# Kernel tuning notes

Hardware: AMD Instinct MI355X
Metric: run time of the kernel (lower is better)

The kernel has to match this reference:

```python
import jax, jax.numpy as jnp
import numpy as np

SEQ, BATCH = 1024, 2
N_HEAD, D_MODEL = 16, 1024
Q_LORA, KV_LORA = 20, 20
ROPE = D_MODEL // N_HEAD // 2   # 32 qk_rope_head_dim
NOPE = D_MODEL // N_HEAD // 2   # 32 qk_nope_head_dim
V_DIM = D_MODEL // N_HEAD       # 64
N_EXP, HID = 4, 1024            # hidden_dim = d_inner//5 = 5120//5
N_GROUP, TOPK_GROUP, TOP_K = 2, 2, 1
ROUTED_SCALE = 1.0


def setup_inputs() -> dict:
    key = jax.random.key(0)
    ks = jax.random.split(key, 16)
    sc = 0.02
    return {
        'dec_inp': jax.random.normal(ks[0], (SEQ, BATCH, D_MODEL), jnp.float32),
        'wq_a': jax.random.normal(ks[1], (D_MODEL, Q_LORA), jnp.float32) * sc,
        'q_norm_w': jnp.ones((Q_LORA,), jnp.float32),
        'wq_b': jax.random.normal(ks[2], (Q_LORA, N_HEAD * (NOPE + ROPE)), jnp.float32) * sc,
        'wkv_a': jax.random.normal(ks[3], (D_MODEL, KV_LORA + ROPE), jnp.float32) * sc,
        'kv_norm_w': jnp.ones((KV_LORA,), jnp.float32),
        'wkv_b': jax.random.normal(ks[4], (KV_LORA, N_HEAD * (NOPE + V_DIM)), jnp.float32) * sc,
        'wo': jax.random.normal(ks[5], (N_HEAD * V_DIM, D_MODEL), jnp.float32) * sc,
        'gate_w': jax.random.normal(ks[6], (N_EXP, D_MODEL), jnp.float32) * sc,
        'exp_gate': jax.random.normal(ks[7], (N_EXP, D_MODEL, HID), jnp.float32) * sc,
        'exp_up': jax.random.normal(ks[8], (N_EXP, D_MODEL, HID), jnp.float32) * sc,
        'exp_down': jax.random.normal(ks[9], (N_EXP, HID, D_MODEL), jnp.float32) * sc,
        'sh_gate': jax.random.normal(ks[10], (D_MODEL, HID), jnp.float32) * sc,
        'sh_up': jax.random.normal(ks[11], (D_MODEL, HID), jnp.float32) * sc,
        'sh_down': jax.random.normal(ks[12], (HID, D_MODEL), jnp.float32) * sc,
    }


def _rms(x, w, eps=1e-6):
    return x * jax.lax.rsqrt(jnp.mean(x * x, axis=-1, keepdims=True) + eps) * w


def _freqs(seqlen):
    # precompute_freqs_cis(rope_dim * n_head, seqlen): dim = 512 here
    dim = ROPE * N_HEAD
    inv = 1.0 / (10000.0 ** (jnp.arange(0, dim, 2, dtype=jnp.float32) / dim))  # [dim//2]
    ang = jnp.arange(seqlen, dtype=jnp.float32)[:, None] * inv[None, :]       # [s, dim//2]
    ang = ang.reshape(seqlen, N_HEAD, ROPE // 2)
    return jnp.cos(ang), jnp.sin(ang)


def _rope(x, cos, sin):
    # x: [b, s, h, ROPE]; interleaved-pair complex rotation
    b, s, h, _ = x.shape
    xr = x.reshape(b, s, h, ROPE // 2, 2)
    x0, x1 = xr[..., 0], xr[..., 1]
    c = cos[None]  # [1, s, h, ROPE//2]
    sn = sin[None]
    o0 = x0 * c - x1 * sn
    o1 = x0 * sn + x1 * c
    return jnp.stack([o0, o1], axis=-1).reshape(b, s, h, ROPE)


def reference(dec_inp, wq_a, q_norm_w, wq_b, wkv_a, kv_norm_w, wkv_b, wo,
              gate_w, exp_gate, exp_up, exp_down, sh_gate, sh_up, sh_down):
    x = jnp.swapaxes(dec_inp, 0, 1)  # [b, s, d]
    b, s, d = x.shape
    # ---- MLA attention ----
    q = _rms(x @ wq_a, q_norm_w) @ wq_b                       # [b, s, h*(nope+rope)]
    q = q.reshape(b, s, N_HEAD, NOPE + ROPE)
    q_nope, q_pe = q[..., :NOPE], q[..., NOPE:]
    kv = x @ wkv_a                                            # [b, s, kv_lora+rope]
    ckv, k_pe = kv[..., :KV_LORA], kv[..., KV_LORA:]
    kvb = (_rms(ckv, kv_norm_w) @ wkv_b).reshape(b, s, N_HEAD, NOPE + V_DIM)
    k_nope, v = kvb[..., :NOPE], kvb[..., NOPE:]
    cos, sin = _freqs(s)
    q_pe = _rope(q_pe, cos, sin)
    k_pe_h = _rope(jnp.broadcast_to(k_pe[:, :, None, :], (b, s, N_HEAD, ROPE)), cos, sin)
    qf = jnp.concatenate([q_nope, q_pe], axis=-1)             # [b, s, h, 64]
    kf = jnp.concatenate([k_nope, k_pe_h], axis=-1)
    scale = 1.0 / np.sqrt(NOPE + ROPE)
    scores = jnp.einsum('bshd,bthd->bhst', qf, kf) * scale    # mask=None in the source forward
    probs = jax.nn.softmax(scores, axis=-1)
    attn = jnp.einsum('bhst,bthd->bshd', probs, v).reshape(b, s, N_HEAD * V_DIM)
    y = attn @ wo                                             # [b, s, d]
    y = jnp.swapaxes(y, 0, 1)                                 # [s, b, d]
    # ---- DeepSeekMoE (group_limited_greedy, top_k=1, 1 shared expert) ----
    xf = y.reshape(-1, d)                                     # [T, d]
    T = xf.shape[0]
    sc = jax.nn.softmax(xf @ gate_w.T, axis=-1)               # [T, E]
    gsc = sc.reshape(T, N_GROUP, N_EXP // N_GROUP).max(axis=-1)  # [T, n_group]
    _, gidx = jax.lax.top_k(gsc, TOPK_GROUP)
    gmask = jax.nn.one_hot(gidx, N_GROUP, dtype=sc.dtype).sum(axis=1)  # [T, n_group]
    smask = jnp.repeat(gmask, N_EXP // N_GROUP, axis=-1)      # [T, E]
    tw, ti = jax.lax.top_k(jnp.where(smask > 0, sc, 0.0), TOP_K)
    comb = (jax.nn.one_hot(ti, N_EXP, dtype=sc.dtype) * tw[..., None]).sum(axis=1) * ROUTED_SCALE  # [T, E]
    g = jnp.einsum('td,edh->teh', xf, exp_gate)
    u = jnp.einsum('td,edh->teh', xf, exp_up)
    dn = jnp.einsum('teh,ehd->ted', jax.nn.silu(g) * u, exp_down)
    routed = jnp.einsum('ted,te->td', dn, comb)
    shared = (jax.nn.silu(xf @ sh_gate) * (xf @ sh_up)) @ sh_down
    return (routed + shared).reshape(s, b, d)
```

## Files before the change

### kernel.cpp

```cpp
#include <hip/hip_runtime.h>
#include <hip/hip_bf16.h>
#include <math.h>

#define SEQ 1024
#define BATCH 2
#define T 2048
#define DM 1024
#define NH 16
#define NOPE 32
#define HD 64
#define QL 20
#define KVL 20
#define KVA 52
#define HID 1024
#define NEXP 4
#define LSTR 80

typedef short bf16x8 __attribute__((ext_vector_type(8)));
typedef float f32x4 __attribute__((ext_vector_type(4)));
typedef float f32x16 __attribute__((ext_vector_type(16)));
typedef __hip_bfloat16 bf16;

static __device__ __forceinline__ float sigmoidf_(float x) {
    return 1.0f / (1.0f + __expf(-x));
}
static __device__ __forceinline__ unsigned short bfbits(float x) {
    bf16 h = __float2bfloat16(x);
    return *reinterpret_cast<unsigned short*>(&h);
}
static __device__ __forceinline__ unsigned cvt_pk_bf16(float lo, float hi) {
    unsigned r;
    asm("v_cvt_pk_bf16_f32 %0, %1, %2" : "=v"(r) : "v"(lo), "v"(hi));
    return r;
}

__global__ __launch_bounds__(256) void k_setup(
    const float* __restrict__ wo, const float* __restrict__ sg,
    const float* __restrict__ su, const float* __restrict__ sd,
    const float* __restrict__ eg, const float* __restrict__ eu,
    const float* __restrict__ ed,
    bf16* __restrict__ woT, bf16* __restrict__ sgT, bf16* __restrict__ suT,
    bf16* __restrict__ sdT, bf16* __restrict__ egT, bf16* __restrict__ euT,
    bf16* __restrict__ edT,
    const float* __restrict__ wq_a, const float* __restrict__ wkv_a,
    const float* __restrict__ wq_b, const float* __restrict__ wkv_b,
    bf16* __restrict__ loraT, bf16* __restrict__ wqbT, bf16* __restrict__ wkvbT,
    float* __restrict__ ctab, float* __restrict__ stab)
{
    int z = blockIdx.z;
    int tid = threadIdx.x;
    if (z < 16) {
        __shared__ float tile[32][33];
        const float* in; bf16* out;
        if      (z == 0) { in = wo; out = woT; }
        else if (z == 1) { in = sg; out = sgT; }
        else if (z == 2) { in = su; out = suT; }
        else if (z == 3) { in = sd; out = sdT; }
        else if (z < 8)  { size_t o = (size_t)(z - 4)  * DM * HID; in = eg + o; out = egT + o; }
        else if (z < 12) { size_t o = (size_t)(z - 8)  * DM * HID; in = eu + o; out = euT + o; }
        else             { size_t o = (size_t)(z - 12) * HID * DM; in = ed + o; out = edT + o; }
        int c0 = blockIdx.x * 32, r0 = blockIdx.y * 32;
        int tx = tid & 31, ty = tid >> 5;
        #pragma unroll
        for (int ii = 0; ii < 4; ++ii)
            tile[ty + ii * 8][tx] = in[(size_t)(r0 + ty + ii * 8) * 1024 + c0 + tx];
        __syncthreads();
        int c = tid >> 3, rg = (tid & 7) * 4;
        ushort4 o4;
        o4.x = bfbits(tile[rg + 0][c]);
        o4.y = bfbits(tile[rg + 1][c]);
        o4.z = bfbits(tile[rg + 2][c]);
        o4.w = bfbits(tile[rg + 3][c]);
        *(ushort4*)&out[(size_t)(c0 + c) * 1024 + r0 + rg] = o4;
    } else if (z == 16) {
        int s = blockIdx.y * 32 + blockIdx.x;
        int p = tid;
        float freq = exp2f(-(float)p * (13.287712379549449f / 256.0f));
        float ang = (float)s * freq;
        float sn, cs;
        __sincosf(ang, &sn, &cs);
        ctab[s * 256 + p] = cs;
        stab[s * 256 + p] = sn;
    } else {
        int idx = (blockIdx.y * 32 + blockIdx.x) * 256 + tid;
        if (z == 17) {
            if (idx >= 80 * 1024) return;
            int n = idx >> 10, k = idx & 1023;
            float v = (n < 20) ? wq_a[k * QL + n] : (n < 72 ? wkv_a[k * KVA + (n - 20)] : 0.f);
            loraT[idx] = __float2bfloat16(v);
        } else if (z == 18) {
            if (idx >= 1024 * 32) return;
            int n = idx >> 5, k = idx & 31;
            wqbT[idx] = __float2bfloat16(k < 20 ? wq_b[k * DM + n] : 0.f);
        } else {
            if (idx >= 1536 * 32) return;
            int n = idx >> 5, k = idx & 31;
            wkvbT[idx] = __float2bfloat16(k < 20 ? wkv_b[k * (NH * 96) + n] : 0.f);
        }
    }
}

__global__ __launch_bounds__(256) void k_p1(
    const float* __restrict__ dec, const bf16* __restrict__ loraT,
    float* __restrict__ lora4)
{
    __shared__ __align__(16) char As[128 * LSTR];
    __shared__ __align__(16) char Bs[80 * LSTR];
    const int tid = threadIdx.x;
    const int kz = blockIdx.x;
    const int m0 = blockIdx.y * 128;
    const int lane = tid & 63, wave = tid >> 6;
    const int g = lane >> 4, c = lane & 15;
    f32x4 acc[2][5] = {};
    for (int ks = 0; ks < 16; ++ks) {
        int k0 = kz * 512 + ks * 32;
        __syncthreads();
        #pragma unroll
        for (int pass = 0; pass < 4; ++pass) {
            int row = (tid >> 3) + pass * 32;
            int t = m0 + row;
            int b = t >> 10, s = t & 1023;
            f32x4 v = *(const f32x4*)&dec[(size_t)(s * 2 + b) * DM + k0 + (tid & 7) * 4];
            ushort4 h4;
            h4.x = bfbits(v[0]); h4.y = bfbits(v[1]);
            h4.z = bfbits(v[2]); h4.w = bfbits(v[3]);
            *(ushort4*)&As[row * LSTR + (tid & 7) * 8] = h4;
        }
        if (tid < 160) {
            int row = tid >> 1, hf = tid & 1;
            const bf16* src = &loraT[row * 1024 + k0 + hf * 16];
            *(int4*)&Bs[row * LSTR + hf * 32]      = *(const int4*)&src[0];
            *(int4*)&Bs[row * LSTR + hf * 32 + 16] = *(const int4*)&src[8];
        }
        __syncthreads();
        bf16x8 af[2], bff[5];
        #pragma unroll
        for (int mi = 0; mi < 2; ++mi)
            af[mi] = *(const bf16x8*)&As[(wave * 32 + mi * 16 + c) * LSTR + 16 * g];
        #pragma unroll
        for (int nf = 0; nf < 5; ++nf)
            bff[nf] = *(const bf16x8*)&Bs[(nf * 16 + c) * LSTR + 16 * g];
        #pragma unroll
        for (int mi = 0; mi < 2; ++mi)
            #pragma unroll
            for (int nf = 0; nf < 5; ++nf)
                acc[mi][nf] = __builtin_amdgcn_mfma_f32_16x16x32_bf16(af[mi], bff[nf], acc[mi][nf], 0, 0, 0);
    }
    #pragma unroll
    for (int mi = 0; mi < 2; ++mi)
        #pragma unroll
        for (int nf = 0; nf < 5; ++nf)
            #pragma unroll
            for (int r = 0; r < 4; ++r) {
                int col = nf * 16 + c;
                if (col < 72) {
                    int row = m0 + wave * 32 + mi * 16 + 4 * g + r;
                    lora4[((size_t)kz * T + row) * 72 + col] = acc[mi][nf][r];
                }
            }
}

__global__ __launch_bounds__(256) void k_p2(
    const float* __restrict__ lora4, const float* __restrict__ qnw,
    const float* __restrict__ kvnw, bf16* __restrict__ nrmq, bf16* __restrict__ nrmkv,
    int* __restrict__ cnt)
{
    if (blockIdx.x == 0 && threadIdx.x < 16) cnt[threadIdx.x] = 0;
    int t = blockIdx.x * 256 + threadIdx.x;
    float lq[20], lk[20];
    float ssq = 0.f, ssk = 0.f;
    #pragma unroll
    for (int i = 0; i < 20; ++i) {
        lq[i] = lora4[t * 72 + i] + lora4[(size_t)(T + t) * 72 + i];
        ssq += lq[i] * lq[i];
    }
    #pragma unroll
    for (int i = 0; i < 20; ++i) {
        lk[i] = lora4[t * 72 + 20 + i] + lora4[(size_t)(T + t) * 72 + 20 + i];
        ssk += lk[i] * lk[i];
    }
    float fq = rsqrtf(ssq / 20.f + 1e-6f);
    float fk = rsqrtf(ssk / 20.f + 1e-6f);
    #pragma unroll
    for (int i = 0; i < 32; ++i) {
        nrmq[t * 32 + i]  = __float2bfloat16(i < 20 ? lq[i] * fq * qnw[i]  : 0.f);
        nrmkv[t * 32 + i] = __float2bfloat16(i < 20 ? lk[i] * fk * kvnw[i] : 0.f);
    }
}

__global__ __launch_bounds__(256) void k_p2b(
    const float* __restrict__ lora4, const float* __restrict__ ctab,
    const float* __restrict__ stab, bf16* __restrict__ kb)
{
    int t = blockIdx.x, p = threadIdx.x;
    int r = p & 15, h = p >> 4, s = t & (SEQ - 1);
    float y0 = lora4[t * 72 + 40 + 2 * r] + lora4[(size_t)(T + t) * 72 + 40 + 2 * r];
    float y1 = lora4[t * 72 + 41 + 2 * r] + lora4[(size_t)(T + t) * 72 + 41 + 2 * r];
    float cs = ctab[s * 256 + p], sn = stab[s * 256 + p];
    ushort2 pk;
    pk.x = bfbits(y0 * cs - y1 * sn);
    pk.y = bfbits(y0 * sn + y1 * cs);
    *(ushort2*)&kb[(size_t)t * DM + h * HD + NOPE + 2 * r] = pk;
}

__global__ __launch_bounds__(256) void k_p3q(
    const bf16* __restrict__ nrmq, const bf16* __restrict__ wqbT,
    const float* __restrict__ ctab, const float* __restrict__ stab,
    bf16* __restrict__ qb)
{
    __shared__ __align__(16) char As[128 * LSTR];
    __shared__ __align__(16) char Bs[64 * LSTR];
    const int tid = threadIdx.x;
    const int m0 = blockIdx.y * 128, n0 = blockIdx.x * 64;
    const int lane = tid & 63, wave = tid >> 6;
    const int g = lane >> 4, c = lane & 15;
    const int wm = wave >> 1, wn = wave & 1;
    {
        int row = tid >> 1, hf = tid & 1;
        const bf16* sa = &nrmq[(size_t)(m0 + row) * 32 + hf * 16];
        *(int4*)&As[row * LSTR + hf * 32]      = *(const int4*)&sa[0];
        *(int4*)&As[row * LSTR + hf * 32 + 16] = *(const int4*)&sa[8];
        int brow = tid >> 2;
        *(int4*)&Bs[brow * LSTR + (tid & 3) * 16] = *(const int4*)&wqbT[(size_t)(n0 + brow) * 32 + (tid & 3) * 8];
    }
    __syncthreads();
    f32x4 acc[4][2] = {};
    bf16x8 af[4], bfr[2];
    #pragma unroll
    for (int mi = 0; mi < 4; ++mi)
        af[mi] = *(const bf16x8*)&As[(wm * 64 + mi * 16 + c) * LSTR + 16 * g];
    #pragma unroll
    for (int ni = 0; ni < 2; ++ni)
        bfr[ni] = *(const bf16x8*)&Bs[(wn * 32 + ni * 16 + c) * LSTR + 16 * g];
    #pragma unroll
    for (int mi = 0; mi < 4; ++mi)
        #pragma unroll
        for (int ni = 0; ni < 2; ++ni) {
            acc[mi][ni] = __builtin_amdgcn_mfma_f32_16x16x32_bf16(af[mi], bfr[ni], acc[mi][ni], 0, 0, 0);
            #pragma unroll
            for (int r = 0; r < 4; ++r) acc[mi][ni][r] *= 0.18033688f;
        }

    #pragma unroll
    for (int mi = 0; mi < 4; ++mi)
        #pragma unroll
        for (int ni = 0; ni < 2; ++ni) {
            int n = n0 + wn * 32 + ni * 16 + c;
            int w = n & 63;
            if (w < 32) {
                #pragma unroll
                for (int r = 0; r < 4; ++r) {
                    int row = m0 + wm * 64 + mi * 16 + 4 * g + r;
                    qb[(size_t)row * DM + n] = __float2bfloat16(acc[mi][ni][r]);
                }
            } else {
                int h = n >> 6;
                int pidx = h * 16 + ((w - 32) >> 1);
                int odd = w & 1;
                #pragma unroll
                for (int r = 0; r < 4; ++r) {
                    int row = m0 + wm * 64 + mi * 16 + 4 * g + r;
                    int s = row & (SEQ - 1);
                    float own = acc[mi][ni][r];
                    float oth = __shfl_xor(own, 1);
                    float cs = ctab[s * 256 + pidx], sn = stab[s * 256 + pidx];
                    float o = odd ? (oth * sn + own * cs) : (own * cs - oth * sn);
                    qb[(size_t)row * DM + n] = __float2bfloat16(o);
                }
            }
        }
}

__global__ __launch_bounds__(256) void k_p3kv(
    const bf16* __restrict__ nrmkv, const bf16* __restrict__ wkvbT,
    bf16* __restrict__ kb, bf16* __restrict__ vt_g)
{
    __shared__ __align__(16) char As[128 * LSTR];
    __shared__ __align__(16) char Bs[64 * LSTR];
    const int tid = threadIdx.x;
    const int m0 = blockIdx.y * 128, n0 = blockIdx.x * 64;
    const int lane = tid & 63, wave = tid >> 6;
    const int g = lane >> 4, c = lane & 15;
    const int wm = wave >> 1, wn = wave & 1;
    {
        int row = tid >> 1, hf = tid & 1;
        const bf16* sa = &nrmkv[(size_t)(m0 + row) * 32 + hf * 16];
        *(int4*)&As[row * LSTR + hf * 32]      = *(const int4*)&sa[0];
        *(int4*)&As[row * LSTR + hf * 32 + 16] = *(const int4*)&sa[8];
        int brow = tid >> 2;
        *(int4*)&Bs[brow * LSTR + (tid & 3) * 16] = *(const int4*)&wkvbT[(size_t)(n0 + brow) * 32 + (tid & 3) * 8];
    }
    __syncthreads();
    f32x4 acc[4][2] = {};
    bf16x8 af[4], bfr[2];
    #pragma unroll
    for (int mi = 0; mi < 4; ++mi)
        af[mi] = *(const bf16x8*)&As[(wm * 64 + mi * 16 + c) * LSTR + 16 * g];
    #pragma unroll
    for (int ni = 0; ni < 2; ++ni)
        bfr[ni] = *(const bf16x8*)&Bs[(wn * 32 + ni * 16 + c) * LSTR + 16 * g];
    #pragma unroll
    for (int mi = 0; mi < 4; ++mi)
        #pragma unroll
        for (int ni = 0; ni < 2; ++ni)
            acc[mi][ni] = __builtin_amdgcn_mfma_f32_16x16x32_bf16(af[mi], bfr[ni], acc[mi][ni], 0, 0, 0);

    #pragma unroll
    for (int mi = 0; mi < 4; ++mi)
        #pragma unroll
        for (int ni = 0; ni < 2; ++ni) {
            int n = n0 + wn * 32 + ni * 16 + c;
            int h = n / 96, w = n - h * 96;
            int row0 = m0 + wm * 64 + mi * 16 + 4 * g;
            if (w < NOPE) {
                #pragma unroll
                for (int r = 0; r < 4; ++r)
                    kb[(size_t)(row0 + r) * DM + h * HD + w] = __float2bfloat16(acc[mi][ni][r]);
            } else {
                int d = w - NOPE;
                int b = row0 >> 10, s0 = row0 & (SEQ - 1);
                ushort4 v4;
                v4.x = bfbits(acc[mi][ni][0]);
                v4.y = bfbits(acc[mi][ni][1]);
                v4.z = bfbits(acc[mi][ni][2]);
                v4.w = bfbits(acc[mi][ni][3]);
                *(ushort4*)&vt_g[(((size_t)(b * NH + h) * HD + d) << 10) + s0] = v4;
            }
        }
}

__global__ __launch_bounds__(256) void k_attn(
    const bf16* __restrict__ qb, const bf16* __restrict__ kb,
    const bf16* __restrict__ vt_g, bf16* __restrict__ ab)
{
    __shared__ __align__(16) char stage[2][16384];
    __shared__ float pol[2][32][65];
    __shared__ float mll[2][32][2];

    const int qt = blockIdx.x, h = blockIdx.y, b = blockIdx.z;
    const int tid = threadIdx.x;
    const int lane = tid & 63, wave = tid >> 6;
    const int l31 = lane & 31, hi = lane >> 5;
    const int sp = wave >> 1, wq = wave & 1;
    const int q0 = qt * 64 + wq * 32;
    char* ks = stage[sp];
    char* vt = stage[sp] + 8192;
    const int ptid = tid & 127;

    bf16x8 qf[4];
    {
        const bf16* qrow = &qb[(size_t)(b * SEQ + q0 + l31) * DM + h * HD + 8 * hi];
        #pragma unroll
        for (int st = 0; st < 4; ++st)
            qf[st] = *(const bf16x8*)&qrow[16 * st];
    }

    f32x16 o0 = {}, o1 = {};
    float m_run = -3.0e38f, l_run = 0.f;
    const size_t vbase = ((size_t)(b * NH + h) * HD) << 10;

    for (int ktl = 0; ktl < 8; ++ktl) {
        const int kt = sp * 8 + ktl;
        __syncthreads();
        #pragma unroll
        for (int ps = 0; ps < 4; ++ps) {
            int row = (ptid >> 3) + ps * 16;
            int col8 = (ptid & 7) * 8;
            int sw = (col8 * 2) ^ ((row & 7) << 4);
            int4 kv4 = *(const int4*)&kb[(size_t)(b * SEQ + kt * 64 + row) * DM + h * HD + col8];
            *(int4*)&ks[row * 128 + sw] = kv4;
            int4 vv4 = *(const int4*)&vt_g[vbase + ((size_t)row << 10) + kt * 64 + col8];
            *(int4*)&vt[row * 128 + sw] = vv4;
        }
        __syncthreads();

        f32x16 sc0 = {}, sc1 = {};
        #pragma unroll
        for (int st = 0; st < 4; ++st) {
            int colb = 32 * st + 16 * hi;
            int r0 = l31;
            bf16x8 kf0 = *(const bf16x8*)&ks[r0 * 128 + (colb ^ ((r0 & 7) << 4))];
            sc0 = __builtin_amdgcn_mfma_f32_32x32x16_bf16(kf0, qf[st], sc0, 0, 0, 0);
            int r1 = 32 + l31;
            bf16x8 kf1 = *(const bf16x8*)&ks[r1 * 128 + (colb ^ ((r1 & 7) << 4))];
            sc1 = __builtin_amdgcn_mfma_f32_32x32x16_bf16(kf1, qf[st], sc1, 0, 0, 0);
        }

        float mt = fmaxf(sc0[0], sc1[0]);
        #pragma unroll
        for (int i = 1; i < 16; ++i) mt = fmaxf(mt, fmaxf(sc0[i], sc1[i]));
        mt = fmaxf(mt, __shfl_xor(mt, 32));

        if (!__all(mt <= m_run + 8.0f)) {
            float m_new = fmaxf(m_run, mt);
            float corr = exp2f(m_run - m_new);
            m_run = m_new;
            l_run *= corr;
            #pragma unroll
            for (int i = 0; i < 16; ++i) { o0[i] *= corr; o1[i] *= corr; }
        }
        float ls = 0.f;
        #pragma unroll
        for (int i = 0; i < 16; ++i) {
            sc0[i] = exp2f(sc0[i] - m_run);
            sc1[i] = exp2f(sc1[i] - m_run);
            ls += sc0[i] + sc1[i];
        }
        ls += __shfl_xor(ls, 32);
        l_run += ls;

        unsigned pk0[8], pk1[8];
        #pragma unroll
        for (int i = 0; i < 8; ++i) {
            pk0[i] = cvt_pk_bf16(sc0[2 * i], sc0[2 * i + 1]);
            pk1[i] = cvt_pk_bf16(sc1[2 * i], sc1[2 * i + 1]);
        }

#define PV_SUB(PK, KK)                                                          \
        {                                                                       \
            _Pragma("unroll")                                                   \
            for (int s = 0; s < 2; ++s) {                                       \
                unsigned sx = hi ? PK[4*s]   : PK[4*s+2];                       \
                unsigned rx = __shfl_xor(sx, 32);                               \
                unsigned sy = hi ? PK[4*s+1] : PK[4*s+3];                       \
                unsigned ry = __shfl_xor(sy, 32);                               \
                int4 bi;                                                        \
                bi.x = hi ? (int)rx : (int)PK[4*s];                             \
                bi.y = hi ? (int)ry : (int)PK[4*s+1];                           \
                bi.z = hi ? (int)PK[4*s+2] : (int)rx;                           \
                bi.w = hi ? (int)PK[4*s+3] : (int)ry;                           \
                bf16x8 bfr = *(bf16x8*)&bi;                                     \
                int cb = (KK) * 64 + 32 * s + 16 * hi;                          \
                {                                                               \
                    int vr = l31;                                               \
                    bf16x8 vf = *(const bf16x8*)&vt[vr * 128 + (cb ^ ((vr & 7) << 4))]; \
                    o0 = __builtin_amdgcn_mfma_f32_32x32x16_bf16(vf, bfr, o0, 0, 0, 0); \
                }                                                               \
                {                                                               \
                    int vr = 32 + l31;                                          \
                    bf16x8 vf = *(const bf16x8*)&vt[vr * 128 + (cb ^ ((vr & 7) << 4))]; \
                    o1 = __builtin_amdgcn_mfma_f32_32x32x16_bf16(vf, bfr, o1, 0, 0, 0); \
                }                                                               \
            }                                                                   \
        }
        PV_SUB(pk0, 0)
        PV_SUB(pk1, 1)
#undef PV_SUB
    }

    if (sp == 1) {
        #pragma unroll
        for (int i = 0; i < 16; ++i) {
            int d = (i & 3) + 8 * (i >> 2) + 4 * hi;
            pol[wq][l31][d]      = o0[i];
            pol[wq][l31][32 + d] = o1[i];
        }
        if (hi == 0) { mll[wq][l31][0] = m_run; mll[wq][l31][1] = l_run; }
    }
    __syncthreads();
    if (sp == 1) return;

    float m_b = mll[wq][l31][0], l_b = mll[wq][l31][1];
    float M = fmaxf(m_run, m_b);
    float wa = exp2f(m_run - M), wb = exp2f(m_b - M);
    float inv = 1.0f / (l_run * wa + l_b * wb);
    #pragma unroll
    for (int i = 0; i < 16; ++i) {
        int d = (i & 3) + 8 * (i >> 2) + 4 * hi;
        o0[i] = (o0[i] * wa + pol[wq][l31][d]      * wb) * inv;
        o1[i] = (o1[i] * wa + pol[wq][l31][32 + d] * wb) * inv;
    }

    char* tb = stage[wq];
    #pragma unroll
    for (int i = 0; i < 8; ++i) {
        int dbase = 2 * (i & 1) + 8 * (i >> 1) + 4 * hi;
        *(unsigned*)&tb[l31 * 140 + (dbase) * 2]      = cvt_pk_bf16(o0[2 * i], o0[2 * i + 1]);
        *(unsigned*)&tb[l31 * 140 + (32 + dbase) * 2] = cvt_pk_bf16(o1[2 * i], o1[2 * i + 1]);
    }
    __builtin_amdgcn_s_waitcnt(0);
    #pragma unroll
    for (int p = 0; p < 8; ++p) {
        int idx = p * 64 + lane;
        int q = idx >> 4, c8 = idx & 15;
        int2 rv;
        rv.x = *(const int*)&tb[q * 140 + c8 * 8];
        rv.y = *(const int*)&tb[q * 140 + c8 * 8 + 4];
        *(int2*)&ab[(size_t)(b * SEQ + q0 + q) * DM + h * HD + c8 * 4] = rv;
    }
}

__global__ __launch_bounds__(512) void k_mm_plain(
    const bf16* __restrict__ A, const bf16* __restrict__ Bt, bf16* __restrict__ C)
{
    __shared__ __align__(16) char As[128 * LSTR];
    __shared__ __align__(16) char Bs[64 * LSTR];
    const int tid = threadIdx.x;
    const int lane = tid & 63, wave = tid >> 6;
    const int g = lane >> 4, c = lane & 15;
    const int wm = wave >> 1, wn = wave & 1;
    const int m0 = blockIdx.y * 128, n0 = blockIdx.x * 64;
    const int sr = tid >> 2, sb = (tid & 3) * 16, scol = (tid & 3) * 8;
    const int srb = (tid & 255) >> 2;

    size_t aoff = (size_t)(m0 + sr) * DM + scol;
    size_t boff = (size_t)(n0 + srb) * DM + scol;
    int4 a0 = *(const int4*)&A[aoff];
    int4 b0;
    if (tid < 256) b0 = *(const int4*)&Bt[boff];

    f32x4 acc[2][2] = {};
    for (int k0 = 0; k0 < DM; k0 += 32) {
        __syncthreads();
        *(int4*)&As[sr * LSTR + sb] = a0;
        if (tid < 256) *(int4*)&Bs[srb * LSTR + sb] = b0;
        __syncthreads();
        if (k0 + 32 < DM) {
            a0 = *(const int4*)&A[aoff + k0 + 32];
            if (tid < 256) b0 = *(const int4*)&Bt[boff + k0 + 32];
        }
        bf16x8 af[2], bfx[2];
        #pragma unroll
        for (int mi = 0; mi < 2; ++mi)
            af[mi] = *(const bf16x8*)&As[(wm * 32 + mi * 16 + c) * LSTR + 16 * g];
        #pragma unroll
        for (int ni = 0; ni < 2; ++ni)
            bfx[ni] = *(const bf16x8*)&Bs[(wn * 32 + ni * 16 + c) * LSTR + 16 * g];
        #pragma unroll
        for (int mi = 0; mi < 2; ++mi)
            #pragma unroll
            for (int ni = 0; ni < 2; ++ni)
                acc[mi][ni] = __builtin_amdgcn_mfma_f32_16x16x32_bf16(af[mi], bfx[ni], acc[mi][ni], 0, 0, 0);
    }
    #pragma unroll
    for (int mi = 0; mi < 2; ++mi)
        #pragma unroll
        for (int ni = 0; ni < 2; ++ni)
            #pragma unroll
            for (int r = 0; r < 4; ++r)
                C[(size_t)(m0 + wm * 32 + mi * 16 + 4 * g + r) * DM + n0 + wn * 32 + ni * 16 + c]
                    = __float2bfloat16(acc[mi][ni][r]);
}

template<bool ROUTED>
__global__ __launch_bounds__(512) void k_mm_gu(
    const bf16* __restrict__ X, const bf16* __restrict__ BgT,
    const bf16* __restrict__ BuT, const int* __restrict__ cnt,
    const int* __restrict__ lists, bf16* __restrict__ act)
{
    const int e = blockIdx.z;
    const int ntok = ROUTED ? cnt[e] : T;
    const int m0 = blockIdx.y * 128;
    if (m0 >= ntok) return;
    const int n0 = blockIdx.x * 64;
    __shared__ __align__(16) char As[128 * LSTR];
    __shared__ __align__(16) char Bg[64 * LSTR];
    __shared__ __align__(16) char Bu[64 * LSTR];
    __shared__ int rowid[128];
    const int tid = threadIdx.x;
    if (tid < 128) {
        int idx = m0 + tid;
        rowid[tid] = ROUTED ? lists[e * T + (idx < ntok ? idx : ntok - 1)] : idx;
    }
    __syncthreads();
    const int lane = tid & 63, wave = tid >> 6;
    const int g = lane >> 4, c = lane & 15;
    const int wm = wave >> 1, wn = wave & 1;
    const int sr = tid >> 2, sb = (tid & 3) * 16, scol = (tid & 3) * 8;
    const int srb = (tid & 255) >> 2;
    const int ra = rowid[sr];
    const bf16* Bge = BgT + (ROUTED ? (size_t)e * HID * DM : 0);
    const bf16* Bue = BuT + (ROUTED ? (size_t)e * HID * DM : 0);
    const bf16* Bmine = (tid < 256) ? Bge : Bue;
    size_t aoff = (size_t)ra * DM + scol;
    size_t boff = (size_t)(n0 + srb) * DM + scol;
    int4 a0 = *(const int4*)&X[aoff];
    int4 b0 = *(const int4*)&Bmine[boff];
    char* Bdst = (tid < 256) ? Bg : Bu;

    f32x4 accg[2][2] = {}, accu[2][2] = {};
    for (int k0 = 0; k0 < DM; k0 += 32) {
        __syncthreads();
        *(int4*)&As[sr * LSTR + sb] = a0;
        *(int4*)&Bdst[srb * LSTR + sb] = b0;
        __syncthreads();
        if (k0 + 32 < DM) {
            a0 = *(const int4*)&X[aoff + k0 + 32];
            b0 = *(const int4*)&Bmine[boff + k0 + 32];
        }
        bf16x8 af[2], gf[2], uf[2];
        #pragma unroll
        for (int mi = 0; mi < 2; ++mi)
            af[mi] = *(const bf16x8*)&As[(wm * 32 + mi * 16 + c) * LSTR + 16 * g];
        #pragma unroll
        for (int ni = 0; ni < 2; ++ni) {
            gf[ni] = *(const bf16x8*)&Bg[(wn * 32 + ni * 16 + c) * LSTR + 16 * g];
            uf[ni] = *(const bf16x8*)&Bu[(wn * 32 + ni * 16 + c) * LSTR + 16 * g];
        }
        #pragma unroll
        for (int mi = 0; mi < 2; ++mi)
            #pragma unroll
            for (int ni = 0; ni < 2; ++ni) {
                accg[mi][ni] = __builtin_amdgcn_mfma_f32_16x16x32_bf16(af[mi], gf[ni], accg[mi][ni], 0, 0, 0);
                accu[mi][ni] = __builtin_amdgcn_mfma_f32_16x16x32_bf16(af[mi], uf[ni], accu[mi][ni], 0, 0, 0);
            }
    }
    #pragma unroll
    for (int mi = 0; mi < 2; ++mi)
        #pragma unroll
        for (int ni = 0; ni < 2; ++ni)
            #pragma unroll
            for (int r = 0; r < 4; ++r) {
                int lr = wm * 32 + mi * 16 + 4 * g + r;
                if (ROUTED && m0 + lr >= ntok) continue;
                int token = rowid[lr];
                float gv = accg[mi][ni][r], uv = accu[mi][ni][r];
                act[(size_t)token * HID + n0 + wn * 32 + ni * 16 + c] =
                    __float2bfloat16(gv * sigmoidf_(gv) * uv);
            }
}

template<bool ROUTED>
__global__ __launch_bounds__(512) void k_mm_down(
    const bf16* __restrict__ Xact, const bf16* __restrict__ BdT,
    const int* __restrict__ cnt, const int* __restrict__ lists,
    const float* __restrict__ wtok, float* __restrict__ out)
{
    const int e = blockIdx.z;
    const int ntok = ROUTED ? cnt[e] : T;
    const int m0 = blockIdx.y * 128;
    if (m0 >= ntok) return;
    const int n0 = blockIdx.x * 64;
    __shared__ __align__(16) char As[128 * LSTR];
    __shared__ __align__(16) char Bs[64 * LSTR];
    __shared__ int rowid[128];
    const int tid = threadIdx.x;
    if (tid < 128) {
        int idx = m0 + tid;
        rowid[tid] = ROUTED ? lists[e * T + (idx < ntok ? idx : ntok - 1)] : idx;
    }
    __syncthreads();
    const int lane = tid & 63, wave = tid >> 6;
    const int g = lane >> 4, c = lane & 15;
    const int wm = wave >> 1, wn = wave & 1;
    const int sr = tid >> 2, sb = (tid & 3) * 16, scol = (tid & 3) * 8;
    const int srb = (tid & 255) >> 2;
    const int ra = rowid[sr];
    const bf16* Bde = BdT + (ROUTED ? (size_t)e * HID * DM : 0);
    size_t aoff = (size_t)ra * HID + scol;
    size_t boff = (size_t)(n0 + srb) * HID + scol;
    int4 a0 = *(const int4*)&Xact[aoff];
    int4 b0;
    if (tid < 256) b0 = *(const int4*)&Bde[boff];

    f32x4 acc[2][2] = {};
    for (int k0 = 0; k0 < HID; k0 += 32) {
        __syncthreads();
        *(int4*)&As[sr * LSTR + sb] = a0;
        if (tid < 256) *(int4*)&Bs[srb * LSTR + sb] = b0;
        __syncthreads();
        if (k0 + 32 < HID) {
            a0 = *(const int4*)&Xact[aoff + k0 + 32];
            if (tid < 256) b0 = *(const int4*)&Bde[boff + k0 + 32];
        }
        bf16x8 af[2], bfx[2];
        #pragma unroll
        for (int mi = 0; mi < 2; ++mi)
            af[mi] = *(const bf16x8*)&As[(wm * 32 + mi * 16 + c) * LSTR + 16 * g];
        #pragma unroll
        for (int ni = 0; ni < 2; ++ni)
            bfx[ni] = *(const bf16x8*)&Bs[(wn * 32 + ni * 16 + c) * LSTR + 16 * g];
        #pragma unroll
        for (int mi = 0; mi < 2; ++mi)
            #pragma unroll
            for (int ni = 0; ni < 2; ++ni)
                acc[mi][ni] = __builtin_amdgcn_mfma_f32_16x16x32_bf16(af[mi], bfx[ni], acc[mi][ni], 0, 0, 0);
    }
    #pragma unroll
    for (int mi = 0; mi < 2; ++mi)
        #pragma unroll
        for (int ni = 0; ni < 2; ++ni)
            #pragma unroll
            for (int r = 0; r < 4; ++r) {
                int lr = wm * 32 + mi * 16 + 4 * g + r;
                if (ROUTED && m0 + lr >= ntok) continue;
                int token = rowid[lr];
                int bt = token >> 10, st = token & (SEQ - 1);
                size_t oo = (size_t)st * (BATCH * DM) + bt * DM + n0 + wn * 32 + ni * 16 + c;
                if (ROUTED) out[oo] = acc[mi][ni][r] * wtok[token];
                else        out[oo] += acc[mi][ni][r];
            }
}

__global__ __launch_bounds__(256) void k_gate(
    const bf16* __restrict__ y, const float* __restrict__ gw,
    int* __restrict__ cnt, int* __restrict__ lists, float* __restrict__ wtok)
{
    int warp = threadIdx.x >> 6, lane = threadIdx.x & 63;
    int t = blockIdx.x * 4 + warp;
    float acc[NEXP] = {};
    for (int d = lane; d < DM; d += 64) {
        float xv = __bfloat162float(y[(size_t)t * DM + d]);
        #pragma unroll
        for (int e = 0; e < NEXP; ++e) acc[e] += xv * gw[e * DM + d];
    }
    #pragma unroll
    for (int off = 32; off; off >>= 1)
        #pragma unroll
        for (int e = 0; e < NEXP; ++e) acc[e] += __shfl_xor(acc[e], off);
    if (lane == 0) {
        float mx = fmaxf(fmaxf(acc[0], acc[1]), fmaxf(acc[2], acc[3]));
        float ex[NEXP], ssum = 0.f;
        #pragma unroll
        for (int e = 0; e < NEXP; ++e) { ex[e] = __expf(acc[e] - mx); ssum += ex[e]; }
        int best = 0; float bv = ex[0];
        #pragma unroll
        for (int e = 1; e < NEXP; ++e) if (ex[e] > bv) { bv = ex[e]; best = e; }
        wtok[t] = bv / ssum;
        int pos = atomicAdd(&cnt[best], 1);
        lists[best * T + pos] = t;
    }
}

extern "C" void kernel_launch(void* const* d_in, const int* in_sizes, int n_in,
                              void* d_out, int out_size, void* d_ws, size_t ws_size,
                              hipStream_t stream) {
    (void)in_sizes; (void)n_in; (void)out_size; (void)ws_size;
    const float* dec      = (const float*)d_in[0];
    const float* wq_a     = (const float*)d_in[1];
    const float* q_norm_w = (const float*)d_in[2];
    const float* wq_b     = (const float*)d_in[3];
    const float* wkv_a    = (const float*)d_in[4];
    const float* kv_norm_w= (const float*)d_in[5];
    const float* wkv_b    = (const float*)d_in[6];
    const float* wo       = (const float*)d_in[7];
    const float* gate_w   = (const float*)d_in[8];
    const float* exp_gate = (const float*)d_in[9];
    const float* exp_up   = (const float*)d_in[10];
    const float* exp_down = (const float*)d_in[11];
    const float* sh_gate  = (const float*)d_in[12];
    const float* sh_up    = (const float*)d_in[13];
    const float* sh_down  = (const float*)d_in[14];
    float* out = (float*)d_out;

    char* W = (char*)d_ws;
    bf16* qb   = (bf16*)(W);
    bf16* kb   = (bf16*)(W + (4ull  << 20));
    bf16* vt_g = (bf16*)(W + (8ull  << 20));
    char* SMALL = W + (12ull << 20);
    bf16* ab   = (bf16*)(W + (12ull << 20));
    bf16* woT = (bf16*)(W + (16ull << 20));
    bf16* sgT = (bf16*)(W + (18ull << 20));
    bf16* suT = (bf16*)(W + (20ull << 20));
    bf16* sdT = (bf16*)(W + (22ull << 20));
    bf16* egT = (bf16*)(W + (24ull << 20));
    bf16* euT = (bf16*)(W + (32ull << 20));
    bf16* edT = (bf16*)(W + (40ull << 20));
    int*   cnt   = (int*)(W + (48ull << 20));
    int*   lists = cnt + 16;
    float* wtok  = (float*)(lists + NEXP * T);
    bf16* yb    = qb;
    bf16* act_r = kb;
    bf16* act_s = vt_g;

    float* lora4 = (float*)(SMALL);
    bf16*  loraT = (bf16*) (SMALL + 1179648);
    bf16*  wqbT  = (bf16*) (SMALL + 1343488);
    bf16*  wkvbT = (bf16*) (SMALL + 1409024);
    bf16*  nrmq  = (bf16*) (SMALL + 1507328);
    bf16*  nrmkv = (bf16*) (SMALL + 1638400);
    float* ctab  = (float*)(SMALL + 1769472);
    float* stab  = (float*)(SMALL + 2818048);

    k_setup<<<dim3(32, 32, 20), 256, 0, stream>>>(
        wo, sh_gate, sh_up, sh_down, exp_gate, exp_up, exp_down,
        woT, sgT, suT, sdT, egT, euT, edT,
        wq_a, wkv_a, wq_b, wkv_b, loraT, wqbT, wkvbT, ctab, stab);

    k_p1<<<dim3(2, 16), 256, 0, stream>>>(dec, loraT, lora4);
    k_p2<<<T / 256, 256, 0, stream>>>(lora4, q_norm_w, kv_norm_w, nrmq, nrmkv, cnt);
    k_p2b<<<T, 256, 0, stream>>>(lora4, ctab, stab, kb);
    k_p3q<<<dim3(16, 16), 256, 0, stream>>>(nrmq, wqbT, ctab, stab, qb);
    k_p3kv<<<dim3(24, 16), 256, 0, stream>>>(nrmkv, wkvbT, kb, vt_g);

    k_attn<<<dim3(SEQ / 64, NH, BATCH), 256, 0, stream>>>(qb, kb, vt_g, ab);
    k_mm_plain<<<dim3(DM / 64, T / 128), 512, 0, stream>>>(ab, woT, yb);
    k_gate<<<T / 4, 256, 0, stream>>>(yb, gate_w, cnt, lists, wtok);
    k_mm_gu<true><<<dim3(HID / 64, T / 128, NEXP), 512, 0, stream>>>(yb, egT, euT, cnt, lists, act_r);
    k_mm_down<true><<<dim3(DM / 64, T / 128, NEXP), 512, 0, stream>>>(act_r, edT, cnt, lists, wtok, out);
    k_mm_gu<false><<<dim3(HID / 64, T / 128, 1), 512, 0, stream>>>(yb, sgT, suT, cnt, lists, act_s);
    k_mm_down<false><<<dim3(DM / 64, T / 128, 1), 512, 0, stream>>>(act_s, sdT, cnt, lists, wtok, out);
}
```

Before: 205.9 us.

## Double-buffer GEMMs with direct global-to-LDS loads and merge shared gate/up launch

The three bf16 MFMA GEMM kernels (wo projection, expert gate/up, down) now use global_load_lds to copy tiles straight into double-buffered LDS with explicit vmcnt waits, instead of staging them through registers with two syncthreads per k-step. The routed and shared-expert gate/up GEMMs are merged into one launch with a fifth z-slice for the shared expert, which removes a launch and lets the two fill the GPU together. The LDS layout drops its padding (64-byte row stride), which may add bank conflicts, and the hand-counted vmcnt values must match the issued loads for correctness.

```diff
diff --git a/kernel.cpp b/kernel.cpp
--- a/kernel.cpp
+++ b/kernel.cpp
@@ -33,6 +33,17 @@
     asm("v_cvt_pk_bf16_f32 %0, %1, %2" : "=v"(r) : "v"(lo), "v"(hi));
     return r;
 }
+static __device__ __forceinline__ void gload16(const bf16* g, char* l) {
+    __builtin_amdgcn_global_load_lds(
+        (const __attribute__((address_space(1))) unsigned int*)g,
+        (__attribute__((address_space(3))) unsigned int*)l, 16, 0, 0);
+}
+static __device__ __forceinline__ void barrier_() {
+    asm volatile("" ::: "memory");
+    __builtin_amdgcn_s_barrier();
+    asm volatile("" ::: "memory");
+}
+#define VMWAIT(N) asm volatile("s_waitcnt vmcnt(" #N ")" ::: "memory")
 
 __global__ __launch_bounds__(256) void k_setup(
     const float* __restrict__ wo, const float* __restrict__ sg,
@@ -493,44 +504,48 @@
 __global__ __launch_bounds__(512) void k_mm_plain(
     const bf16* __restrict__ A, const bf16* __restrict__ Bt, bf16* __restrict__ C)
 {
-    __shared__ __align__(16) char As[128 * LSTR];
-    __shared__ __align__(16) char Bs[64 * LSTR];
+    __shared__ __align__(16) char As[2][8192];
+    __shared__ __align__(16) char Bs[2][4096];
     const int tid = threadIdx.x;
     const int lane = tid & 63, wave = tid >> 6;
     const int g = lane >> 4, c = lane & 15;
     const int wm = wave >> 1, wn = wave & 1;
     const int m0 = blockIdx.y * 128, n0 = blockIdx.x * 64;
-    const int sr = tid >> 2, sb = (tid & 3) * 16, scol = (tid & 3) * 8;
-    const int srb = (tid & 255) >> 2;
-
-    size_t aoff = (size_t)(m0 + sr) * DM + scol;
-    size_t boff = (size_t)(n0 + srb) * DM + scol;
-    int4 a0 = *(const int4*)&A[aoff];
-    int4 b0;
-    if (tid < 256) b0 = *(const int4*)&Bt[boff];
+
+    const int ldr = lane >> 2;
+    const int ldc = (lane & 3) * 8;
+    const bf16* agp = &A[(size_t)(m0 + wave * 16 + ldr) * DM + ldc];
+    const bool doB = wave >= 4;
+    const bf16* bgp = &Bt[(size_t)(n0 + (wave & 3) * 16 + ldr) * DM + ldc];
+    const int aoffL = wave * 1024, boffL = (wave & 3) * 1024;
 
     f32x4 acc[2][2] = {};
-    for (int k0 = 0; k0 < DM; k0 += 32) {
-        __syncthreads();
-        *(int4*)&As[sr * LSTR + sb] = a0;
-        if (tid < 256) *(int4*)&Bs[srb * LSTR + sb] = b0;
-        __syncthreads();
-        if (k0 + 32 < DM) {
-            a0 = *(const int4*)&A[aoff + k0 + 32];
-            if (tid < 256) b0 = *(const int4*)&Bt[boff + k0 + 32];
-        }
+    const int NT = DM / 32;
+    gload16(agp, As[0] + aoffL);
+    if (doB) gload16(bgp, Bs[0] + boffL);
+    for (int k = 0; k < NT; ++k) {
+        const int cur = k & 1;
+        if (k + 1 < NT) {
+            gload16(agp + (k + 1) * 32, As[cur ^ 1] + aoffL);
+            if (doB) gload16(bgp + (k + 1) * 32, Bs[cur ^ 1] + boffL);
+            if (doB) VMWAIT(2); else VMWAIT(1);
+        } else {
+            VMWAIT(0);
+        }
+        barrier_();
         bf16x8 af[2], bfx[2];
         #pragma unroll
         for (int mi = 0; mi < 2; ++mi)
-            af[mi] = *(const bf16x8*)&As[(wm * 32 + mi * 16 + c) * LSTR + 16 * g];
+            af[mi] = *(const bf16x8*)&As[cur][(wm * 32 + mi * 16 + c) * 64 + g * 16];
         #pragma unroll
         for (int ni = 0; ni < 2; ++ni)
-            bfx[ni] = *(const bf16x8*)&Bs[(wn * 32 + ni * 16 + c) * LSTR + 16 * g];
+            bfx[ni] = *(const bf16x8*)&Bs[cur][(wn * 32 + ni * 16 + c) * 64 + g * 16];
         #pragma unroll
         for (int mi = 0; mi < 2; ++mi)
             #pragma unroll
             for (int ni = 0; ni < 2; ++ni)
                 acc[mi][ni] = __builtin_amdgcn_mfma_f32_16x16x32_bf16(af[mi], bfx[ni], acc[mi][ni], 0, 0, 0);
+        barrier_();
     }
     #pragma unroll
     for (int mi = 0; mi < 2; ++mi)
@@ -542,20 +557,104 @@
                     = __float2bfloat16(acc[mi][ni][r]);
 }
 
+__global__ __launch_bounds__(512) void k_mm_gu_all(
+    const bf16* __restrict__ X, const bf16* __restrict__ egT,
+    const bf16* __restrict__ euT, const bf16* __restrict__ sgT,
+    const bf16* __restrict__ suT, const int* __restrict__ cnt,
+    const int* __restrict__ lists, bf16* __restrict__ act_r,
+    bf16* __restrict__ act_s)
+{
+    const int e = blockIdx.z;
+    const bool SH = (e == 4);
+    const int ntok = SH ? T : cnt[e];
+    const int m0 = blockIdx.y * 128;
+    if (m0 >= ntok) return;
+    const int n0 = blockIdx.x * 64;
+    __shared__ __align__(16) char As[2][8192];
+    __shared__ __align__(16) char Bg[2][4096];
+    __shared__ __align__(16) char Bu[2][4096];
+    __shared__ int rowid[128];
+    const int tid = threadIdx.x;
+    if (tid < 128) {
+        int idx = m0 + tid;
+        rowid[tid] = SH ? idx : lists[e * T + (idx < ntok ? idx : ntok - 1)];
+    }
+    __syncthreads();
+    const int lane = tid & 63, wave = tid >> 6;
+    const int g = lane >> 4, c = lane & 15;
+    const int wm = wave >> 1, wn = wave & 1;
+    const bf16* Bge = SH ? sgT : egT + (size_t)e * HID * DM;
+    const bf16* Bue = SH ? suT : euT + (size_t)e * HID * DM;
+    bf16* act = SH ? act_s : act_r;
+
+    const int ldr = lane >> 2;
+    const int ldc = (lane & 3) * 8;
+    const int myTok = rowid[wave * 16 + ldr];
+    const bf16* agp = &X[(size_t)myTok * DM + ldc];
+    const bool isG = wave < 4;
+    const bf16* bgp = (isG ? Bge : Bue) + (size_t)(n0 + (wave & 3) * 16 + ldr) * DM + ldc;
+    const int aoffL = wave * 1024, boffL = (wave & 3) * 1024;
+
+    f32x4 accg[2][2] = {}, accu[2][2] = {};
+    const int NT = DM / 32;
+    gload16(agp, As[0] + aoffL);
+    gload16(bgp, (isG ? Bg[0] : Bu[0]) + boffL);
+    for (int k = 0; k < NT; ++k) {
+        const int cur = k & 1;
+        if (k + 1 < NT) {
+            gload16(agp + (k + 1) * 32, As[cur ^ 1] + aoffL);
+            gload16(bgp + (k + 1) * 32, (isG ? Bg[cur ^ 1] : Bu[cur ^ 1]) + boffL);
+            VMWAIT(2);
+        } else {
+            VMWAIT(0);
+        }
+        barrier_();
+        bf16x8 af[2], gf[2], uf[2];
+        #pragma unroll
+        for (int mi = 0; mi < 2; ++mi)
+            af[mi] = *(const bf16x8*)&As[cur][(wm * 32 + mi * 16 + c) * 64 + g * 16];
+        #pragma unroll
+        for (int ni = 0; ni < 2; ++ni) {
+            gf[ni] = *(const bf16x8*)&Bg[cur][(wn * 32 + ni * 16 + c) * 64 + g * 16];
+            uf[ni] = *(const bf16x8*)&Bu[cur][(wn * 32 + ni * 16 + c) * 64 + g * 16];
+        }
+        #pragma unroll
+        for (int mi = 0; mi < 2; ++mi)
+            #pragma unroll
+            for (int ni = 0; ni < 2; ++ni) {
+                accg[mi][ni] = __builtin_amdgcn_mfma_f32_16x16x32_bf16(af[mi], gf[ni], accg[mi][ni], 0, 0, 0);
+                accu[mi][ni] = __builtin_amdgcn_mfma_f32_16x16x32_bf16(af[mi], uf[ni], accu[mi][ni], 0, 0, 0);
+            }
+        barrier_();
+    }
+    #pragma unroll
+    for (int mi = 0; mi < 2; ++mi)
+        #pragma unroll
+        for (int ni = 0; ni < 2; ++ni)
+            #pragma unroll
+            for (int r = 0; r < 4; ++r) {
+                int lr = wm * 32 + mi * 16 + 4 * g + r;
+                if (!SH && m0 + lr >= ntok) continue;
+                int token = rowid[lr];
+                float gv = accg[mi][ni][r], uv = accu[mi][ni][r];
+                act[(size_t)token * HID + n0 + wn * 32 + ni * 16 + c] =
+                    __float2bfloat16(gv * sigmoidf_(gv) * uv);
+            }
+}
+
 template<bool ROUTED>
-__global__ __launch_bounds__(512) void k_mm_gu(
-    const bf16* __restrict__ X, const bf16* __restrict__ BgT,
-    const bf16* __restrict__ BuT, const int* __restrict__ cnt,
-    const int* __restrict__ lists, bf16* __restrict__ act)
+__global__ __launch_bounds__(512) void k_mm_down(
+    const bf16* __restrict__ Xact, const bf16* __restrict__ BdT,
+    const int* __restrict__ cnt, const int* __restrict__ lists,
+    const float* __restrict__ wtok, float* __restrict__ out)
 {
     const int e = blockIdx.z;
     const int ntok = ROUTED ? cnt[e] : T;
     const int m0 = blockIdx.y * 128;
     if (m0 >= ntok) return;
     const int n0 = blockIdx.x * 64;
-    __shared__ __align__(16) char As[128 * LSTR];
-    __shared__ __align__(16) char Bg[64 * LSTR];
-    __shared__ __align__(16) char Bu[64 * LSTR];
+    __shared__ __align__(16) char As[2][8192];
+    __shared__ __align__(16) char Bs[2][4096];
     __shared__ int rowid[128];
     const int tid = threadIdx.x;
     if (tid < 128) {
@@ -566,115 +665,43 @@
     const int lane = tid & 63, wave = tid >> 6;
     const int g = lane >> 4, c = lane & 15;
     const int wm = wave >> 1, wn = wave & 1;
-    const int sr = tid >> 2, sb = (tid & 3) * 16, scol = (tid & 3) * 8;
-    const int srb = (tid & 255) >> 2;
-    const int ra = rowid[sr];
-    const bf16* Bge = BgT + (ROUTED ? (size_t)e * HID * DM : 0);
-    const bf16* Bue = BuT + (ROUTED ? (size_t)e * HID * DM : 0);
-    const bf16* Bmine = (tid < 256) ? Bge : Bue;
-    size_t aoff = (size_t)ra * DM + scol;
-    size_t boff = (size_t)(n0 + srb) * DM + scol;
-    int4 a0 = *(const int4*)&X[aoff];
-    int4 b0 = *(const int4*)&Bmine[boff];
-    char* Bdst = (tid < 256) ? Bg : Bu;
-
-    f32x4 accg[2][2] = {}, accu[2][2] = {};
-    for (int k0 = 0; k0 < DM; k0 += 32) {
-        __syncthreads();
-        *(int4*)&As[sr * LSTR + sb] = a0;
-        *(int4*)&Bdst[srb * LSTR + sb] = b0;
-        __syncthreads();
-        if (k0 + 32 < DM) {
-            a0 = *(const int4*)&X[aoff + k0 + 32];
-            b0 = *(const int4*)&Bmine[boff + k0 + 32];
-        }
-        bf16x8 af[2], gf[2], uf[2];
+    const bf16* Bde = BdT + (ROUTED ? (size_t)e * HID * DM : 0);
+
+    const int ldr = lane >> 2;
+    const int ldc = (lane & 3) * 8;
+    const int myTok = rowid[wave * 16 + ldr];
+    const bf16* agp = &Xact[(size_t)myTok * HID + ldc];
+    const bool doB = wave >= 4;
+    const bf16* bgp = &Bde[(size_t)(n0 + (wave & 3) * 16 + ldr) * HID + ldc];
+    const int aoffL = wave * 1024, boffL = (wave & 3) * 1024;
+
+    f32x4 acc[2][2] = {};
+    const int NT = HID / 32;
+    gload16(agp, As[0] + aoffL);
+    if (doB) gload16(bgp, Bs[0] + boffL);
+    for (int k = 0; k < NT; ++k) {
+        const int cur = k & 1;
+        if (k + 1 < NT) {
+            gload16(agp + (k + 1) * 32, As[cur ^ 1] + aoffL);
+            if (doB) gload16(bgp + (k + 1) * 32, Bs[cur ^ 1] + boffL);
+            if (doB) VMWAIT(2); else VMWAIT(1);
+        } else {
+            VMWAIT(0);
+        }
+        barrier_();
+        bf16x8 af[2], bfx[2];
         #pragma unroll
         for (int mi = 0; mi < 2; ++mi)
-            af[mi] = *(const bf16x8*)&As[(wm * 32 + mi * 16 + c) * LSTR + 16 * g];
-        #pragma unroll
-        for (int ni = 0; ni < 2; ++ni) {
-            gf[ni] = *(const bf16x8*)&Bg[(wn * 32 + ni * 16 + c) * LSTR + 16 * g];
-            uf[ni] = *(const bf16x8*)&Bu[(wn * 32 + ni * 16 + c) * LSTR + 16 * g];
-        }
-        #pragma unroll
-        for (int mi = 0; mi < 2; ++mi)
-            #pragma unroll
-            for (int ni = 0; ni < 2; ++ni) {
-                accg[mi][ni] = __builtin_amdgcn_mfma_f32_16x16x32_bf16(af[mi], gf[ni], accg[mi][ni], 0, 0, 0);
-                accu[mi][ni] = __builtin_amdgcn_mfma_f32_16x16x32_bf16(af[mi], uf[ni], accu[mi][ni], 0, 0, 0);
-            }
-    }
-    #pragma unroll
-    for (int mi = 0; mi < 2; ++mi)
+            af[mi] = *(const bf16x8*)&As[cur][(wm * 32 + mi * 16 + c) * 64 + g * 16];
         #pragma unroll
         for (int ni = 0; ni < 2; ++ni)
-            #pragma unroll
-            for (int r = 0; r < 4; ++r) {
-                int lr = wm * 32 + mi * 16 + 4 * g + r;
-                if (ROUTED && m0 + lr >= ntok) continue;
-                int token = rowid[lr];
-                float gv = accg[mi][ni][r], uv = accu[mi][ni][r];
-                act[(size_t)token * HID + n0 + wn * 32 + ni * 16 + c] =
-                    __float2bfloat16(gv * sigmoidf_(gv) * uv);
-            }
-}
-
-template<bool ROUTED>
-__global__ __launch_bounds__(512) void k_mm_down(
-    const bf16* __restrict__ Xact, const bf16* __restrict__ BdT,
-    const int* __restrict__ cnt, const int* __restrict__ lists,
-    const float* __restrict__ wtok, float* __restrict__ out)
-{
-    const int e = blockIdx.z;
-    const int ntok = ROUTED ? cnt[e] : T;
-    const int m0 = blockIdx.y * 128;
-    if (m0 >= ntok) return;
-    const int n0 = blockIdx.x * 64;
-    __shared__ __align__(16) char As[128 * LSTR];
-    __shared__ __align__(16) char Bs[64 * LSTR];
-    __shared__ int rowid[128];
-    const int tid = threadIdx.x;
-    if (tid < 128) {
-        int idx = m0 + tid;
-        rowid[tid] = ROUTED ? lists[e * T + (idx < ntok ? idx : ntok - 1)] : idx;
-    }
-    __syncthreads();
-    const int lane = tid & 63, wave = tid >> 6;
-    const int g = lane >> 4, c = lane & 15;
-    const int wm = wave >> 1, wn = wave & 1;
-    const int sr = tid >> 2, sb = (tid & 3) * 16, scol = (tid & 3) * 8;
-    const int srb = (tid & 255) >> 2;
-    const int ra = rowid[sr];
-    const bf16* Bde = BdT + (ROUTED ? (size_t)e * HID * DM : 0);
-    size_t aoff = (size_t)ra * HID + scol;
-    size_t boff = (size_t)(n0 + srb) * HID + scol;
-    int4 a0 = *(const int4*)&Xact[aoff];
-    int4 b0;
-    if (tid < 256) b0 = *(const int4*)&Bde[boff];
-
-    f32x4 acc[2][2] = {};
-    for (int k0 = 0; k0 < HID; k0 += 32) {
-        __syncthreads();
-        *(int4*)&As[sr * LSTR + sb] = a0;
-        if (tid < 256) *(int4*)&Bs[srb * LSTR + sb] = b0;
-        __syncthreads();
-        if (k0 + 32 < HID) {
-            a0 = *(const int4*)&Xact[aoff + k0 + 32];
-            if (tid < 256) b0 = *(const int4*)&Bde[boff + k0 + 32];
-        }
-        bf16x8 af[2], bfx[2];
-        #pragma unroll
-        for (int mi = 0; mi < 2; ++mi)
-            af[mi] = *(const bf16x8*)&As[(wm * 32 + mi * 16 + c) * LSTR + 16 * g];
-        #pragma unroll
-        for (int ni = 0; ni < 2; ++ni)
-            bfx[ni] = *(const bf16x8*)&Bs[(wn * 32 + ni * 16 + c) * LSTR + 16 * g];
+            bfx[ni] = *(const bf16x8*)&Bs[cur][(wn * 32 + ni * 16 + c) * 64 + g * 16];
         #pragma unroll
         for (int mi = 0; mi < 2; ++mi)
             #pragma unroll
             for (int ni = 0; ni < 2; ++ni)
                 acc[mi][ni] = __builtin_amdgcn_mfma_f32_16x16x32_bf16(af[mi], bfx[ni], acc[mi][ni], 0, 0, 0);
+        barrier_();
     }
     #pragma unroll
     for (int mi = 0; mi < 2; ++mi)
@@ -786,8 +813,8 @@
     k_attn<<<dim3(SEQ / 64, NH, BATCH), 256, 0, stream>>>(qb, kb, vt_g, ab);
     k_mm_plain<<<dim3(DM / 64, T / 128), 512, 0, stream>>>(ab, woT, yb);
     k_gate<<<T / 4, 256, 0, stream>>>(yb, gate_w, cnt, lists, wtok);
-    k_mm_gu<true><<<dim3(HID / 64, T / 128, NEXP), 512, 0, stream>>>(yb, egT, euT, cnt, lists, act_r);
+    k_mm_gu_all<<<dim3(HID / 64, T / 128, NEXP + 1), 512, 0, stream>>>(
+        yb, egT, euT, sgT, suT, cnt, lists, act_r, act_s);
     k_mm_down<true><<<dim3(DM / 64, T / 128, NEXP), 512, 0, stream>>>(act_r, edT, cnt, lists, wtok, out);
-    k_mm_gu<false><<<dim3(HID / 64, T / 128, 1), 512, 0, stream>>>(yb, sgT, suT, cnt, lists, act_s);
     k_mm_down<false><<<dim3(DM / 64, T / 128, 1), 512, 0, stream>>>(act_s, sdT, cnt, lists, wtok, out);
 }
```

Measured after the change: 193.3 us. 6.1% less time.
